# Optimization experiments

Hardware: AMD Instinct MI355X
Metric: run time of the kernel (lower is better)

The kernel has to match this reference:

```python
import jax, jax.numpy as jnp
import numpy as np

MODES, WIDTH, DEPTH, IN_F, OUT_F, HID = 8, 16, 3, 1, 1, 64


def setup_inputs() -> dict:
    key = jax.random.key(0)
    ks = jax.random.split(key, 12)
    B, H, W = 8, 512, 512
    scale = 1.0 / (WIDTH * WIDTH)
    inp = {
        'x': jax.random.normal(ks[0], (B, IN_F, H, W), dtype=jnp.float32),
        'fc0_w': jax.random.normal(ks[1], (IN_F, WIDTH), dtype=jnp.float32) * 0.5,
        'fc0_b': jax.random.normal(ks[2], (WIDTH,), dtype=jnp.float32) * 0.1,
        # complex spectral weights stored as real/imag parts, stacked over depth
        'spec_wr': jax.random.normal(ks[3], (DEPTH, WIDTH, WIDTH, MODES, MODES), dtype=jnp.float32) * scale,
        'spec_wi': jax.random.normal(ks[4], (DEPTH, WIDTH, WIDTH, MODES, MODES), dtype=jnp.float32) * scale,
        # 1x1 convs as [depth, out, in] matmuls + bias
        'conv_w': jax.random.normal(ks[5], (DEPTH, WIDTH, WIDTH), dtype=jnp.float32) * 0.25,
        'conv_b': jax.random.normal(ks[6], (DEPTH, WIDTH), dtype=jnp.float32) * 0.1,
        'fc1_w': jax.random.normal(ks[7], (WIDTH, HID), dtype=jnp.float32) * 0.25,
        'fc1_b': jax.random.normal(ks[8], (HID,), dtype=jnp.float32) * 0.1,
        'fc2_w': jax.random.normal(ks[9], (HID, OUT_F), dtype=jnp.float32) * 0.125,
        'fc2_b': jax.random.normal(ks[10], (OUT_F,), dtype=jnp.float32) * 0.1,
    }
    return inp


def _spectral_conv(x, w):
    # x: [B, Ci, H, W] real; w: [Ci, Co, m, m] complex
    B, C, H, W = x.shape
    m = w.shape[2]
    x_ft = jnp.fft.rfft2(x, norm='forward')  # [B, Ci, H, W//2+1]
    out_modes = jnp.einsum('bixy,ioxy->boxy', x_ft[:, :, :m, :m], w)
    out_ft = jnp.zeros((B, w.shape[1], H, W // 2 + 1), dtype=out_modes.dtype)
    out_ft = out_ft.at[:, :, :m, :m].set(out_modes)
    return jnp.fft.irfft2(out_ft, s=(H, W), norm='forward')


def reference(x, fc0_w, fc0_b, spec_wr, spec_wi, conv_w, conv_b, fc1_w, fc1_b, fc2_w, fc2_b):
    # lift: [B,C,H,W] -> channels-last linear -> [B,width,H,W]
    h = jnp.einsum('bchw,cd->bdhw', x, fc0_w) + fc0_b[None, :, None, None]
    for d in range(DEPTH):
        w_c = (spec_wr[d] + 1j * spec_wi[d]).astype(jnp.complex64)
        y = _spectral_conv(h, w_c)
        local = jnp.einsum('bchw,oc->bohw', h, conv_w[d]) + conv_b[d][None, :, None, None]
        h = y + local
    h = jnp.einsum('bchw,cd->bdhw', h, fc1_w) + fc1_b[None, :, None, None]
    h = jax.nn.relu(h)
    out = jnp.einsum('bchw,cd->bdhw', h, fc2_w) + fc2_b[None, :, None, None]
    return out
```

## Files before the change

kernel.cpp:

```cpp
#include <hip/hip_runtime.h>
#include <math.h>

#define NB 8
#define NH 512
#define NW 512
#define ANG512 0.01227184630308513f
#define SPEC_D 16384

typedef __attribute__((ext_vector_type(8))) _Float16 f16x8;
typedef __attribute__((ext_vector_type(4))) float    f32x4;

__global__ __launch_bounds__(256) void k_pre(const float* __restrict__ x,
                                             float* __restrict__ P) {
    __shared__ float wred[8][16];
    const int tid = threadIdx.x;
    const int w = tid >> 6, lane = tid & 63;
    const int gid = blockIdx.x;
    const int b = gid >> 6, rg = gid & 63;

    #pragma unroll
    for (int rr = 0; rr < 2; ++rr) {
        const int row = rg * 8 + w + 4 * rr;
        const float* xr = x + ((size_t)(b * NH + row)) * NW;

        float p[16];
        #pragma unroll
        for (int j = 0; j < 16; ++j) p[j] = 0.f;

        #pragma unroll
        for (int j = 0; j < 4; ++j) {
            const int ww = lane + (j << 6);
            const float xa = xr[ww], xb = xr[ww + 256];
            const float a = xa + xb, d = xa - xb;
            float c1, s1;
            __sincosf(ANG512 * (float)ww, &s1, &c1);
            p[0] += a;
            p[1] = fmaf(d, c1, p[1]);
            p[9] = fmaf(-d, s1, p[9]);
            const float c2k = 2.f * c1;
            float ckm = 1.f, skm = 0.f, ck = c1, sk = s1;
            #pragma unroll
            for (int k = 2; k < 8; ++k) {
                const float cn = fmaf(c2k, ck, -ckm);
                const float sn = fmaf(c2k, sk, -skm);
                ckm = ck; skm = sk; ck = cn; sk = sn;
                const float v = (k & 1) ? d : a;
                p[k]     = fmaf(v, ck, p[k]);
                p[8 + k] = fmaf(-v, sk, p[8 + k]);
            }
        }
        #pragma unroll
        for (int m = 1; m < 64; m <<= 1) {
            #pragma unroll
            for (int j = 0; j < 16; ++j) p[j] += __shfl_xor(p[j], m);
        }
        if (lane < 16) wred[w + 4 * rr][lane] = p[lane];
    }
    __syncthreads();

    if (tid < 128) {
        const int kx = tid >> 4, q = tid & 15, qm = q & 7;
        float acc = 0.f;
        #pragma unroll
        for (int r = 0; r < 8; ++r) {
            const int row = rg * 8 + r;
            const int m = (kx * row) & 511;
            float cm, s2;
            __sincosf(ANG512 * (float)m, &s2, &cm);
            const float rre = wred[r][qm], rim = wred[r][8 + qm];
            acc += (q < 8) ? (rre * cm + rim * s2)
                           : (rim * cm - rre * s2);
        }
        P[((size_t)((b * 64 + rg) * 8 + kx)) * 16 + q] = acc;
    }
}

__global__ __launch_bounds__(256) void k_modes(
        const float* __restrict__ P,
        const float* __restrict__ spec_wr, const float* __restrict__ spec_wi,
        const float* __restrict__ conv_w, const float* __restrict__ conv_b,
        const float* __restrict__ fc0_w, const float* __restrict__ fc0_b,
        const float* __restrict__ fc1_w, const float* __restrict__ fc1_b,
        float* __restrict__ AH, float* __restrict__ gv, float* __restrict__ Kv) {
    __shared__ __align__(16) float sm[2640];
    float* red2  = sm;
    float* X2    = sm + 256;
    float* Xr    = sm + 272;
    float* Xi    = sm + 400;
    float* Fr    = sm + 528;
    float* Fi    = sm + 656;
    float* Ar    = sm + 784;
    float* Ai    = sm + 912;
    float* Pm    = sm + 1040;
    float* fc1_s = sm + 1552;
    float* ps    = sm + 2576;

    const int tid = threadIdx.x;
    const int bid = blockIdx.x;
    const int b = bid >> 3;
    const int kx = bid & 7;

    {
        const int o = tid >> 4, c = tid & 15;
        float s = 0.f;
        for (int k = 0; k < 16; ++k)
            s += conv_w[512 + o * 16 + k] * conv_w[256 + k * 16 + c];
        Pm[tid] = s;
    }
    Pm[256 + tid] = conv_w[512 + tid];
    #pragma unroll
    for (int k = 0; k < 4; ++k) fc1_s[tid + k * 256] = fc1_w[tid + k * 256];

    {
        const int q = tid & 15, c = tid >> 4;
        float acc = 0.f;
        #pragma unroll
        for (int m = 0; m < 4; ++m) {
            const int rg = c + 16 * m;
            acc += P[((size_t)((b * 64 + rg) * 8 + kx)) * 16 + q];
        }
        red2[c * 16 + q] = acc;
    }
    __syncthreads();
    if (tid < 16) {
        float s = 0.f;
        #pragma unroll
        for (int c = 0; c < 16; ++c) s += red2[c * 16 + tid];
        X2[tid] = s;
    }
    __syncthreads();

    const bool act = (tid < 128);
    const int o = tid >> 3, ky = tid & 7;
    if (act) {
        const float inv = 1.f / (512.f * 512.f);
        float xr0 = fc0_w[o] * X2[ky] * inv;
        float xi0 = fc0_w[o] * X2[8 + ky] * inv;
        if (kx == 0 && ky == 0) xr0 += fc0_b[o];
        Xr[o * 8 + ky] = xr0; Xi[o * 8 + ky] = xi0;
        Ar[o * 8 + ky] = 0.f; Ai[o * 8 + ky] = 0.f;
    }
    __syncthreads();

    for (int dd = 0; dd < 3; ++dd) {
        if (act) {
            float fr = 0.f, fi = 0.f;
            const float* wrp = spec_wr + (size_t)dd * SPEC_D + o * 64 + kx * 8 + ky;
            const float* wip = spec_wi + (size_t)dd * SPEC_D + o * 64 + kx * 8 + ky;
            #pragma unroll
            for (int i = 0; i < 16; ++i) {
                const float wre = wrp[i * 1024];
                const float wim = wip[i * 1024];
                const float xr0 = Xr[i * 8 + ky], xi0 = Xi[i * 8 + ky];
                fr += xr0 * wre - xi0 * wim;
                fi += xr0 * wim + xi0 * wre;
            }
            Fr[o * 8 + ky] = fr; Fi[o * 8 + ky] = fi;
        }
        __syncthreads();
        float xnr = 0.f, xni = 0.f;
        if (act) {
            float ar, ai;
            if (dd == 2) {
                ar = Fr[o * 8 + ky]; ai = Fi[o * 8 + ky];
            } else {
                ar = 0.f; ai = 0.f;
                #pragma unroll
                for (int c = 0; c < 16; ++c) {
                    const float pv = Pm[dd * 256 + o * 16 + c];
                    ar = fmaf(pv, Fr[c * 8 + ky], ar);
                    ai = fmaf(pv, Fi[c * 8 + ky], ai);
                }
            }
            Ar[o * 8 + ky] += ar; Ai[o * 8 + ky] += ai;
            if (dd < 2) {
                const float fr0 = Fr[o * 8 + ky], fi0 = Fi[o * 8 + ky];
                if (ky == 0) {
                    if (kx == 0) { xnr = fr0; xni = 0.f; }
                    else         { xnr = 0.5f * fr0; xni = 0.5f * fi0; }
                } else { xnr = fr0; xni = fi0; }
                #pragma unroll
                for (int c = 0; c < 16; ++c) {
                    const float cc = conv_w[dd * 256 + o * 16 + c];
                    xnr = fmaf(cc, Xr[c * 8 + ky], xnr);
                    xni = fmaf(cc, Xi[c * 8 + ky], xni);
                }
                if (kx == 0 && ky == 0) xnr += conv_b[dd * 16 + o];
            }
        }
        __syncthreads();
        if (act && dd < 2) { Xr[o * 8 + ky] = xnr; Xi[o * 8 + ky] = xni; }
        __syncthreads();
    }

    #pragma unroll
    for (int k2 = 0; k2 < 2; ++k2) {
        const int idx = tid + k2 * 256;
        const int hd = idx >> 3, ky2 = idx & 7;
        float ar = 0.f, ai = 0.f;
        #pragma unroll
        for (int c = 0; c < 16; ++c) {
            const float f = fc1_s[c * 64 + hd];
            ar = fmaf(f, Ar[c * 8 + ky2], ar);
            ai = fmaf(f, Ai[c * 8 + ky2], ai);
        }
        const float ck = (ky2 == 0) ? 1.f : 2.f;
        const size_t off = ((((size_t)(b * 64 + hd)) * 8 + ky2) * 8 + kx) * 2;
        AH[off]     = ck * ar;
        AH[off + 1] = ck * ai;
    }

    if (kx == 0) {
        if (tid < 16) {
            float su = 0.f, sb = 0.f;
            for (int c = 0; c < 16; ++c) {
                su += conv_w[tid * 16 + c] * fc0_w[c];
                sb += conv_w[tid * 16 + c] * fc0_b[c];
            }
            ps[tid] = su; ps[16 + tid] = sb;
        }
        __syncthreads();
        if (tid < 16) {
            float dv = 0.f, ev = conv_b[32 + tid];
            for (int k = 0; k < 16; ++k) {
                dv += Pm[tid * 16 + k] * ps[k];
                ev += Pm[tid * 16 + k] * (ps[16 + k] + conv_b[k]);
                ev += conv_w[512 + tid * 16 + k] * conv_b[16 + k];
            }
            ps[32 + tid] = dv; ps[48 + tid] = ev;
        }
        __syncthreads();
        if (tid < 64) {
            float g = 0.f, K = fc1_b[tid];
            for (int c = 0; c < 16; ++c) {
                g = fmaf(fc1_w[c * 64 + tid], ps[32 + c], g);
                K = fmaf(fc1_w[c * 64 + tid], ps[48 + c], K);
            }
            gv[b * 64 + tid] = g;
            Kv[b * 64 + tid] = K;
        }
    }
}

__global__ __launch_bounds__(256, 4) void k_head(
        const float* __restrict__ x, const float* __restrict__ AH,
        const float* __restrict__ gv, const float* __restrict__ Kv,
        const float* __restrict__ fc2_w, const float* __restrict__ fc2_b,
        float* __restrict__ out) {
    __shared__ __align__(16) _Float16 Ef[2][512][8];
    __shared__ __align__(16) _Float16 Apk[4][4][64][8];

    const int tid  = threadIdx.x;
    const int lane = tid & 63;
    const int rl   = tid >> 6;
    const int b    = blockIdx.x >> 7;
    const int rp   = blockIdx.x & 127;
    const int row  = rp * 4 + rl;

    #pragma unroll
    for (int pxi = 0; pxi < 2; ++pxi) {
        const int px = tid + pxi * 256;
        float c1, s1;
        __sincosf(ANG512 * (float)px, &s1, &c1);
        float ck = 1.f, sk = 0.f;
        #pragma unroll
        for (int k = 0; k < 8; ++k) {
            Ef[0][px][k] = (_Float16)ck;
            Ef[1][px][k] = (_Float16)(-sk);
            const float cn = ck * c1 - sk * s1;
            const float sn = sk * c1 + ck * s1;
            ck = cn; sk = sn;
        }
    }

    float ghr[16], w2r[16];
    {
        const int lg = lane >> 4;
        #pragma unroll
        for (int t = 0; t < 4; ++t)
            #pragma unroll
            for (int v = 0; v < 4; ++v) {
                const int hd = t * 16 + lg * 4 + v;
                ghr[t * 4 + v] = gv[b * 64 + hd];
                w2r[t * 4 + v] = fc2_w[hd];
            }
    }

    {
        float c1, s1;
        __sincosf(ANG512 * (float)row, &s1, &c1);
        float ctr[8], str[8];
        ctr[0] = 1.f; str[0] = 0.f; ctr[1] = c1; str[1] = s1;
        const float c2k = 2.f * c1;
        #pragma unroll
        for (int k = 2; k < 8; ++k) {
            ctr[k] = fmaf(c2k, ctr[k - 1], -ctr[k - 2]);
            str[k] = fmaf(c2k, str[k - 1], -str[k - 2]);
        }
        #pragma unroll
        for (int j = 0; j < 8; ++j) {
            const int idx = lane + j * 64;
            const int hd = idx >> 3, ky = idx & 7;
            const float4* ap = (const float4*)(AH + ((size_t)(b * 64 + hd) * 8 + ky) * 16);
            const float4 a0 = ap[0], a1 = ap[1], a2 = ap[2], a3 = ap[3];
            float wr = a0.x, wi = a0.y;
            wr = fmaf(a0.z, ctr[1], wr); wr = fmaf(-a0.w, str[1], wr);
            wi = fmaf(a0.z, str[1], wi); wi = fmaf(a0.w, ctr[1], wi);
            wr = fmaf(a1.x, ctr[2], wr); wr = fmaf(-a1.y, str[2], wr);
            wi = fmaf(a1.x, str[2], wi); wi = fmaf(a1.y, ctr[2], wi);
            wr = fmaf(a1.z, ctr[3], wr); wr = fmaf(-a1.w, str[3], wr);
            wi = fmaf(a1.z, str[3], wi); wi = fmaf(a1.w, ctr[3], wi);
            wr = fmaf(a2.x, ctr[4], wr); wr = fmaf(-a2.y, str[4], wr);
            wi = fmaf(a2.x, str[4], wi); wi = fmaf(a2.y, ctr[4], wi);
            wr = fmaf(a2.z, ctr[5], wr); wr = fmaf(-a2.w, str[5], wr);
            wi = fmaf(a2.z, str[5], wi); wi = fmaf(a2.w, ctr[5], wi);
            wr = fmaf(a3.x, ctr[6], wr); wr = fmaf(-a3.y, str[6], wr);
            wi = fmaf(a3.x, str[6], wi); wi = fmaf(a3.y, ctr[6], wi);
            wr = fmaf(a3.z, ctr[7], wr); wr = fmaf(-a3.w, str[7], wr);
            wi = fmaf(a3.w, ctr[7], wi); wi = fmaf(a3.z, str[7], wi);
            if (ky == 0) wr += Kv[b * 64 + hd];
            const _Float16 hr  = (_Float16)wr;
            const _Float16 hi_ = (_Float16)wi;
            Apk[rl][0][hd][ky] = hr;
            Apk[rl][1][hd][ky] = hi_;
            Apk[rl][2][hd][ky] = (_Float16)(wr - (float)hr);
            Apk[rl][3][hd][ky] = (_Float16)(wi - (float)hi_);
        }
    }
    __syncthreads();

    f16x8 a1[4];
    {
        const int kb = lane >> 4, m = lane & 15;
        #pragma unroll
        for (int t = 0; t < 4; ++t)
            a1[t] = *(const f16x8*)&Apk[rl][kb][t * 16 + m][0];
    }

    const int eb = (lane >> 4) & 1, n = lane & 15;
    const float fc2b = fc2_b[0];
    const float* xrow = x + ((size_t)(b * NH + row)) * NW;
    float* orow = out + ((size_t)(b * NH + row)) * NW;

    #pragma unroll 2
    for (int pxt = 0; pxt < 32; ++pxt) {
        const int px = pxt * 16 + n;
        const f16x8 b1 = *(const f16x8*)&Ef[eb][px][0];
        f32x4 c[4];
        #pragma unroll
        for (int t = 0; t < 4; ++t) {
            c[t] = (f32x4){0.f, 0.f, 0.f, 0.f};
            c[t] = __builtin_amdgcn_mfma_f32_16x16x32_f16(a1[t], b1, c[t], 0, 0, 0);
        }
        const float xpx = xrow[px];
        float val = 0.f;
        #pragma unroll
        for (int t = 0; t < 4; ++t)
            #pragma unroll
            for (int v = 0; v < 4; ++v) {
                float s = fmaf(ghr[t * 4 + v], xpx, c[t][v]);
                s = fmaxf(s, 0.f);
                val = fmaf(s, w2r[t * 4 + v], val);
            }
        val += __shfl_xor(val, 16);
        val += __shfl_xor(val, 32);
        if (lane < 16) orow[pxt * 16 + lane] = val + fc2b;
    }
}

extern "C" void kernel_launch(void* const* d_in, const int* in_sizes, int n_in,
                              void* d_out, int out_size, void* d_ws, size_t ws_size,
                              hipStream_t stream) {
    const float* x       = (const float*)d_in[0];
    const float* fc0_w   = (const float*)d_in[1];
    const float* fc0_b   = (const float*)d_in[2];
    const float* spec_wr = (const float*)d_in[3];
    const float* spec_wi = (const float*)d_in[4];
    const float* conv_w  = (const float*)d_in[5];
    const float* conv_b  = (const float*)d_in[6];
    const float* fc1_w   = (const float*)d_in[7];
    const float* fc1_b   = (const float*)d_in[8];
    const float* fc2_w   = (const float*)d_in[9];
    const float* fc2_b   = (const float*)d_in[10];
    float* outp = (float*)d_out;

    char* ws = (char*)d_ws;
    float* P  = (float*)ws;
    float* AH = (float*)(ws + 262144);
    float* gv = (float*)(ws + 524288);
    float* Kv = (float*)(ws + 526336);

    k_pre<<<512, 256, 0, stream>>>(x, P);
    k_modes<<<64, 256, 0, stream>>>(P, spec_wr, spec_wi, conv_w, conv_b,
                                    fc0_w, fc0_b, fc1_w, fc1_b, AH, gv, Kv);
    k_head<<<1024, 256, 0, stream>>>(x, AH, gv, Kv, fc2_w, fc2_b, outp);
}
```

Before: 118.0 us.

## Fuse pre-reduction and mode kernels via device-scope atomic counters; prefetch in head

Result: slower. 121.3 us (+2.8%).

```diff
diff --git a/kernel.cpp b/kernel.cpp
--- a/kernel.cpp
+++ b/kernel.cpp
@@ -7,237 +7,266 @@
 #define ANG512 0.01227184630308513f
 #define SPEC_D 16384
 
+#define DEV_SCOPE __HIP_MEMORY_SCOPE_AGENT
+
 typedef __attribute__((ext_vector_type(8))) _Float16 f16x8;
 typedef __attribute__((ext_vector_type(4))) float    f32x4;
 
-__global__ __launch_bounds__(256) void k_pre(const float* __restrict__ x,
-                                             float* __restrict__ P) {
-    __shared__ float wred[8][16];
+__device__ int g_pre[256];
+__device__ int g_done[256];
+
+__global__ __launch_bounds__(256) void k_front(
+        const float* __restrict__ x,
+        const float* __restrict__ spec_wr, const float* __restrict__ spec_wi,
+        const float* __restrict__ conv_w, const float* __restrict__ conv_b,
+        const float* __restrict__ fc0_w, const float* __restrict__ fc0_b,
+        const float* __restrict__ fc1_w, const float* __restrict__ fc1_b,
+        float* __restrict__ P, float* __restrict__ AH,
+        float* __restrict__ gv, float* __restrict__ Kv) {
+    __shared__ __align__(16) float sm[2640];
     const int tid = threadIdx.x;
     const int w = tid >> 6, lane = tid & 63;
     const int gid = blockIdx.x;
     const int b = gid >> 6, rg = gid & 63;
 
-    #pragma unroll
-    for (int rr = 0; rr < 2; ++rr) {
-        const int row = rg * 8 + w + 4 * rr;
-        const float* xr = x + ((size_t)(b * NH + row)) * NW;
-
-        float p[16];
-        #pragma unroll
-        for (int j = 0; j < 16; ++j) p[j] = 0.f;
-
-        #pragma unroll
-        for (int j = 0; j < 4; ++j) {
-            const int ww = lane + (j << 6);
-            const float xa = xr[ww], xb = xr[ww + 256];
-            const float a = xa + xb, d = xa - xb;
-            float c1, s1;
-            __sincosf(ANG512 * (float)ww, &s1, &c1);
-            p[0] += a;
-            p[1] = fmaf(d, c1, p[1]);
-            p[9] = fmaf(-d, s1, p[9]);
-            const float c2k = 2.f * c1;
-            float ckm = 1.f, skm = 0.f, ck = c1, sk = s1;
-            #pragma unroll
-            for (int k = 2; k < 8; ++k) {
-                const float cn = fmaf(c2k, ck, -ckm);
-                const float sn = fmaf(c2k, sk, -skm);
-                ckm = ck; skm = sk; ck = cn; sk = sn;
-                const float v = (k & 1) ? d : a;
-                p[k]     = fmaf(v, ck, p[k]);
-                p[8 + k] = fmaf(-v, sk, p[8 + k]);
-            }
-        }
-        #pragma unroll
-        for (int m = 1; m < 64; m <<= 1) {
-            #pragma unroll
-            for (int j = 0; j < 16; ++j) p[j] += __shfl_xor(p[j], m);
-        }
-        if (lane < 16) wred[w + 4 * rr][lane] = p[lane];
-    }
-    __syncthreads();
-
-    if (tid < 128) {
-        const int kx = tid >> 4, q = tid & 15, qm = q & 7;
-        float acc = 0.f;
-        #pragma unroll
-        for (int r = 0; r < 8; ++r) {
-            const int row = rg * 8 + r;
-            const int m = (kx * row) & 511;
-            float cm, s2;
-            __sincosf(ANG512 * (float)m, &s2, &cm);
-            const float rre = wred[r][qm], rim = wred[r][8 + qm];
-            acc += (q < 8) ? (rre * cm + rim * s2)
-                           : (rim * cm - rre * s2);
-        }
-        P[((size_t)((b * 64 + rg) * 8 + kx)) * 16 + q] = acc;
-    }
-}
-
-__global__ __launch_bounds__(256) void k_modes(
-        const float* __restrict__ P,
-        const float* __restrict__ spec_wr, const float* __restrict__ spec_wi,
-        const float* __restrict__ conv_w, const float* __restrict__ conv_b,
-        const float* __restrict__ fc0_w, const float* __restrict__ fc0_b,
-        const float* __restrict__ fc1_w, const float* __restrict__ fc1_b,
-        float* __restrict__ AH, float* __restrict__ gv, float* __restrict__ Kv) {
-    __shared__ __align__(16) float sm[2640];
-    float* red2  = sm;
-    float* X2    = sm + 256;
-    float* Xr    = sm + 272;
-    float* Xi    = sm + 400;
-    float* Fr    = sm + 528;
-    float* Fi    = sm + 656;
-    float* Ar    = sm + 784;
-    float* Ai    = sm + 912;
-    float* Pm    = sm + 1040;
-    float* fc1_s = sm + 1552;
-    float* ps    = sm + 2576;
-
-    const int tid = threadIdx.x;
-    const int bid = blockIdx.x;
-    const int b = bid >> 3;
-    const int kx = bid & 7;
-
     {
-        const int o = tid >> 4, c = tid & 15;
-        float s = 0.f;
-        for (int k = 0; k < 16; ++k)
-            s += conv_w[512 + o * 16 + k] * conv_w[256 + k * 16 + c];
-        Pm[tid] = s;
-    }
-    Pm[256 + tid] = conv_w[512 + tid];
-    #pragma unroll
-    for (int k = 0; k < 4; ++k) fc1_s[tid + k * 256] = fc1_w[tid + k * 256];
+        float* wred = sm;
+        #pragma unroll
+        for (int rr = 0; rr < 2; ++rr) {
+            const int row = rg * 8 + w + 4 * rr;
+            const float* xr = x + ((size_t)(b * NH + row)) * NW;
+
+            float p[16];
+            #pragma unroll
+            for (int j = 0; j < 16; ++j) p[j] = 0.f;
+
+            #pragma unroll
+            for (int j = 0; j < 4; ++j) {
+                const int ww = lane + (j << 6);
+                const float xa = xr[ww], xb = xr[ww + 256];
+                const float a = xa + xb, d = xa - xb;
+                float c1, s1;
+                __sincosf(ANG512 * (float)ww, &s1, &c1);
+                p[0] += a;
+                p[1] = fmaf(d, c1, p[1]);
+                p[9] = fmaf(-d, s1, p[9]);
+                const float c2k = 2.f * c1;
+                float ckm = 1.f, skm = 0.f, ck = c1, sk = s1;
+                #pragma unroll
+                for (int k = 2; k < 8; ++k) {
+                    const float cn = fmaf(c2k, ck, -ckm);
+                    const float sn = fmaf(c2k, sk, -skm);
+                    ckm = ck; skm = sk; ck = cn; sk = sn;
+                    const float v = (k & 1) ? d : a;
+                    p[k]     = fmaf(v, ck, p[k]);
+                    p[8 + k] = fmaf(-v, sk, p[8 + k]);
+                }
+            }
+            #pragma unroll
+            for (int m = 1; m < 64; m <<= 1) {
+                #pragma unroll
+                for (int j = 0; j < 16; ++j) p[j] += __shfl_xor(p[j], m);
+            }
+            if (lane < 16) wred[(w + 4 * rr) * 16 + lane] = p[lane];
+        }
+        __syncthreads();
+
+        if (tid < 128) {
+            const int kx = tid >> 4, q = tid & 15, qm = q & 15 & 7;
+            float acc = 0.f;
+            #pragma unroll
+            for (int r = 0; r < 8; ++r) {
+                const int row = rg * 8 + r;
+                const int m = (kx * row) & 511;
+                float cm, s2;
+                __sincosf(ANG512 * (float)m, &s2, &cm);
+                const float rre = wred[r * 16 + qm], rim = wred[r * 16 + 8 + qm];
+                acc += (q < 8) ? (rre * cm + rim * s2)
+                               : (rim * cm - rre * s2);
+            }
+            __hip_atomic_store(&P[((size_t)((b * 64 + rg) * 8 + kx)) * 16 + q],
+                               acc, __ATOMIC_RELAXED, DEV_SCOPE);
+        }
+        __syncthreads();
+        if (tid == 0)
+            __hip_atomic_fetch_add(&g_pre[b * 32], 1, __ATOMIC_RELEASE, DEV_SCOPE);
+    }
+
+    if (gid >= 64) return;
 
     {
-        const int q = tid & 15, c = tid >> 4;
-        float acc = 0.f;
-        #pragma unroll
-        for (int m = 0; m < 4; ++m) {
-            const int rg = c + 16 * m;
-            acc += P[((size_t)((b * 64 + rg) * 8 + kx)) * 16 + q];
-        }
-        red2[c * 16 + q] = acc;
-    }
-    __syncthreads();
-    if (tid < 16) {
-        float s = 0.f;
-        #pragma unroll
-        for (int c = 0; c < 16; ++c) s += red2[c * 16 + tid];
-        X2[tid] = s;
-    }
-    __syncthreads();
-
-    const bool act = (tid < 128);
-    const int o = tid >> 3, ky = tid & 7;
-    if (act) {
-        const float inv = 1.f / (512.f * 512.f);
-        float xr0 = fc0_w[o] * X2[ky] * inv;
-        float xi0 = fc0_w[o] * X2[8 + ky] * inv;
-        if (kx == 0 && ky == 0) xr0 += fc0_b[o];
-        Xr[o * 8 + ky] = xr0; Xi[o * 8 + ky] = xi0;
-        Ar[o * 8 + ky] = 0.f; Ai[o * 8 + ky] = 0.f;
-    }
-    __syncthreads();
-
-    for (int dd = 0; dd < 3; ++dd) {
+        float* red2  = sm;
+        float* X2    = sm + 256;
+        float* Xr    = sm + 272;
+        float* Xi    = sm + 400;
+        float* Fr    = sm + 528;
+        float* Fi    = sm + 656;
+        float* Ar    = sm + 784;
+        float* Ai    = sm + 912;
+        float* Pm    = sm + 1040;
+        float* fc1_s = sm + 1552;
+        float* ps    = sm + 2576;
+
+        const int b2 = gid >> 3;
+        const int kx = gid & 7;
+
+        __syncthreads();
+
+        {
+            const int o = tid >> 4, c = tid & 15;
+            float s = 0.f;
+            for (int k = 0; k < 16; ++k)
+                s += conv_w[512 + o * 16 + k] * conv_w[256 + k * 16 + c];
+            Pm[tid] = s;
+        }
+        Pm[256 + tid] = conv_w[512 + tid];
+        #pragma unroll
+        for (int k = 0; k < 4; ++k) fc1_s[tid + k * 256] = fc1_w[tid + k * 256];
+
+        if (tid == 0) {
+            while (__hip_atomic_load(&g_pre[b2 * 32], __ATOMIC_RELAXED, DEV_SCOPE) < 64)
+                __builtin_amdgcn_s_sleep(2);
+        }
+        __syncthreads();
+
+        {
+            const int q = tid & 15, c = tid >> 4;
+            float acc = 0.f;
+            #pragma unroll
+            for (int m = 0; m < 4; ++m) {
+                const int rg2 = c + 16 * m;
+                acc += P[((size_t)((b2 * 64 + rg2) * 8 + kx)) * 16 + q];
+            }
+            red2[c * 16 + q] = acc;
+        }
+        __syncthreads();
+        if (tid < 16) {
+            float s = 0.f;
+            #pragma unroll
+            for (int c = 0; c < 16; ++c) s += red2[c * 16 + tid];
+            X2[tid] = s;
+        }
+        __syncthreads();
+
+        const bool act = (tid < 128);
+        const int o = tid >> 3, ky = tid & 7;
         if (act) {
-            float fr = 0.f, fi = 0.f;
-            const float* wrp = spec_wr + (size_t)dd * SPEC_D + o * 64 + kx * 8 + ky;
-            const float* wip = spec_wi + (size_t)dd * SPEC_D + o * 64 + kx * 8 + ky;
-            #pragma unroll
-            for (int i = 0; i < 16; ++i) {
-                const float wre = wrp[i * 1024];
-                const float wim = wip[i * 1024];
-                const float xr0 = Xr[i * 8 + ky], xi0 = Xi[i * 8 + ky];
-                fr += xr0 * wre - xi0 * wim;
-                fi += xr0 * wim + xi0 * wre;
-            }
-            Fr[o * 8 + ky] = fr; Fi[o * 8 + ky] = fi;
-        }
-        __syncthreads();
-        float xnr = 0.f, xni = 0.f;
-        if (act) {
-            float ar, ai;
-            if (dd == 2) {
-                ar = Fr[o * 8 + ky]; ai = Fi[o * 8 + ky];
-            } else {
-                ar = 0.f; ai = 0.f;
+            const float inv = 1.f / (512.f * 512.f);
+            float xr0 = fc0_w[o] * X2[ky] * inv;
+            float xi0 = fc0_w[o] * X2[8 + ky] * inv;
+            if (kx == 0 && ky == 0) xr0 += fc0_b[o];
+            Xr[o * 8 + ky] = xr0; Xi[o * 8 + ky] = xi0;
+            Ar[o * 8 + ky] = 0.f; Ai[o * 8 + ky] = 0.f;
+        }
+        __syncthreads();
+
+        for (int dd = 0; dd < 3; ++dd) {
+            if (act) {
+                float fr = 0.f, fi = 0.f;
+                const float* wrp = spec_wr + (size_t)dd * SPEC_D + o * 64 + kx * 8 + ky;
+                const float* wip = spec_wi + (size_t)dd * SPEC_D + o * 64 + kx * 8 + ky;
                 #pragma unroll
+                for (int i = 0; i < 16; ++i) {
+                    const float wre = wrp[i * 1024];
+                    const float wim = wip[i * 1024];
+                    const float xr0 = Xr[i * 8 + ky], xi0 = Xi[i * 8 + ky];
+                    fr += xr0 * wre - xi0 * wim;
+                    fi += xr0 * wim + xi0 * wre;
+                }
+                Fr[o * 8 + ky] = fr; Fi[o * 8 + ky] = fi;
+            }
+            __syncthreads();
+            float xnr = 0.f, xni = 0.f;
+            if (act) {
+                float ar, ai;
+                if (dd == 2) {
+                    ar = Fr[o * 8 + ky]; ai = Fi[o * 8 + ky];
+                } else {
+                    ar = 0.f; ai = 0.f;
+                    #pragma unroll
+                    for (int c = 0; c < 16; ++c) {
+                        const float pv = Pm[dd * 256 + o * 16 + c];
+                        ar = fmaf(pv, Fr[c * 8 + ky], ar);
+                        ai = fmaf(pv, Fi[c * 8 + ky], ai);
+                    }
+                }
+                Ar[o * 8 + ky] += ar; Ai[o * 8 + ky] += ai;
+                if (dd < 2) {
+                    const float fr0 = Fr[o * 8 + ky], fi0 = Fi[o * 8 + ky];
+                    if (ky == 0) {
+                        if (kx == 0) { xnr = fr0; xni = 0.f; }
+                        else         { xnr = 0.5f * fr0; xni = 0.5f * fi0; }
+                    } else { xnr = fr0; xni = fi0; }
+                    #pragma unroll
+                    for (int c = 0; c < 16; ++c) {
+                        const float cc = conv_w[dd * 256 + o * 16 + c];
+                        xnr = fmaf(cc, Xr[c * 8 + ky], xnr);
+                        xni = fmaf(cc, Xi[c * 8 + ky], xni);
+                    }
+                    if (kx == 0 && ky == 0) xnr += conv_b[dd * 16 + o];
+                }
+            }
+            __syncthreads();
+            if (act && dd < 2) { Xr[o * 8 + ky] = xnr; Xi[o * 8 + ky] = xni; }
+            __syncthreads();
+        }
+
+        #pragma unroll
+        for (int k2 = 0; k2 < 2; ++k2) {
+            const int idx = tid + k2 * 256;
+            const int hd = idx >> 3, ky2 = idx & 7;
+            float ar = 0.f, ai = 0.f;
+            #pragma unroll
+            for (int c = 0; c < 16; ++c) {
+                const float f = fc1_s[c * 64 + hd];
+                ar = fmaf(f, Ar[c * 8 + ky2], ar);
+                ai = fmaf(f, Ai[c * 8 + ky2], ai);
+            }
+            const float ck = (ky2 == 0) ? 1.f : 2.f;
+            const size_t off = ((((size_t)(b2 * 64 + hd)) * 8 + ky2) * 8 + kx) * 2;
+            AH[off]     = ck * ar;
+            AH[off + 1] = ck * ai;
+        }
+
+        if (kx == 0) {
+            if (tid < 16) {
+                float su = 0.f, sb = 0.f;
                 for (int c = 0; c < 16; ++c) {
-                    const float pv = Pm[dd * 256 + o * 16 + c];
-                    ar = fmaf(pv, Fr[c * 8 + ky], ar);
-                    ai = fmaf(pv, Fi[c * 8 + ky], ai);
-                }
-            }
-            Ar[o * 8 + ky] += ar; Ai[o * 8 + ky] += ai;
-            if (dd < 2) {
-                const float fr0 = Fr[o * 8 + ky], fi0 = Fi[o * 8 + ky];
-                if (ky == 0) {
-                    if (kx == 0) { xnr = fr0; xni = 0.f; }
-                    else         { xnr = 0.5f * fr0; xni = 0.5f * fi0; }
-                } else { xnr = fr0; xni = fi0; }
-                #pragma unroll
+                    su += conv_w[tid * 16 + c] * fc0_w[c];
+                    sb += conv_w[tid * 16 + c] * fc0_b[c];
+                }
+                ps[tid] = su; ps[16 + tid] = sb;
+            }
+            __syncthreads();
+            if (tid < 16) {
+                float dv = 0.f, ev = conv_b[32 + tid];
+                for (int k = 0; k < 16; ++k) {
+                    dv += Pm[tid * 16 + k] * ps[k];
+                    ev += Pm[tid * 16 + k] * (ps[16 + k] + conv_b[k]);
+                    ev += conv_w[512 + tid * 16 + k] * conv_b[16 + k];
+                }
+                ps[32 + tid] = dv; ps[48 + tid] = ev;
+            }
+            __syncthreads();
+            if (tid < 64) {
+                float g = 0.f, K = fc1_b[tid];
                 for (int c = 0; c < 16; ++c) {
-                    const float cc = conv_w[dd * 256 + o * 16 + c];
-                    xnr = fmaf(cc, Xr[c * 8 + ky], xnr);
-                    xni = fmaf(cc, Xi[c * 8 + ky], xni);
-                }
-                if (kx == 0 && ky == 0) xnr += conv_b[dd * 16 + o];
-            }
-        }
-        __syncthreads();
-        if (act && dd < 2) { Xr[o * 8 + ky] = xnr; Xi[o * 8 + ky] = xni; }
-        __syncthreads();
-    }
-
-    #pragma unroll
-    for (int k2 = 0; k2 < 2; ++k2) {
-        const int idx = tid + k2 * 256;
-        const int hd = idx >> 3, ky2 = idx & 7;
-        float ar = 0.f, ai = 0.f;
-        #pragma unroll
-        for (int c = 0; c < 16; ++c) {
-            const float f = fc1_s[c * 64 + hd];
-            ar = fmaf(f, Ar[c * 8 + ky2], ar);
-            ai = fmaf(f, Ai[c * 8 + ky2], ai);
-        }
-        const float ck = (ky2 == 0) ? 1.f : 2.f;
-        const size_t off = ((((size_t)(b * 64 + hd)) * 8 + ky2) * 8 + kx) * 2;
-        AH[off]     = ck * ar;
-        AH[off + 1] = ck * ai;
-    }
-
-    if (kx == 0) {
-        if (tid < 16) {
-            float su = 0.f, sb = 0.f;
-            for (int c = 0; c < 16; ++c) {
-                su += conv_w[tid * 16 + c] * fc0_w[c];
-                sb += conv_w[tid * 16 + c] * fc0_b[c];
-            }
-            ps[tid] = su; ps[16 + tid] = sb;
-        }
-        __syncthreads();
-        if (tid < 16) {
-            float dv = 0.f, ev = conv_b[32 + tid];
-            for (int k = 0; k < 16; ++k) {
-                dv += Pm[tid * 16 + k] * ps[k];
-                ev += Pm[tid * 16 + k] * (ps[16 + k] + conv_b[k]);
-                ev += conv_w[512 + tid * 16 + k] * conv_b[16 + k];
-            }
-            ps[32 + tid] = dv; ps[48 + tid] = ev;
-        }
-        __syncthreads();
-        if (tid < 64) {
-            float g = 0.f, K = fc1_b[tid];
-            for (int c = 0; c < 16; ++c) {
-                g = fmaf(fc1_w[c * 64 + tid], ps[32 + c], g);
-                K = fmaf(fc1_w[c * 64 + tid], ps[48 + c], K);
-            }
-            gv[b * 64 + tid] = g;
-            Kv[b * 64 + tid] = K;
+                    g = fmaf(fc1_w[c * 64 + tid], ps[32 + c], g);
+                    K = fmaf(fc1_w[c * 64 + tid], ps[48 + c], K);
+                }
+                gv[b2 * 64 + tid] = g;
+                Kv[b2 * 64 + tid] = K;
+            }
+        }
+
+        __syncthreads();
+        if (tid == 0) {
+            const int d = __hip_atomic_fetch_add(&g_done[b2 * 32], 1,
+                                                 __ATOMIC_RELAXED, DEV_SCOPE);
+            if (d == 7) {
+                __hip_atomic_store(&g_pre[b2 * 32],  0, __ATOMIC_RELAXED, DEV_SCOPE);
+                __hip_atomic_store(&g_done[b2 * 32], 0, __ATOMIC_RELAXED, DEV_SCOPE);
+            }
         }
     }
 }
@@ -342,17 +371,23 @@
     const float* xrow = x + ((size_t)(b * NH + row)) * NW;
     float* orow = out + ((size_t)(b * NH + row)) * NW;
 
-    #pragma unroll 2
+    f16x8 bnext = *(const f16x8*)&Ef[eb][n][0];
+    float xnext = xrow[n];
+
+    #pragma unroll 4
     for (int pxt = 0; pxt < 32; ++pxt) {
-        const int px = pxt * 16 + n;
-        const f16x8 b1 = *(const f16x8*)&Ef[eb][px][0];
+        const f16x8 b1 = bnext;
+        const float xpx = xnext;
+        if (pxt < 31) {
+            bnext = *(const f16x8*)&Ef[eb][(pxt + 1) * 16 + n][0];
+            xnext = xrow[(pxt + 1) * 16 + n];
+        }
         f32x4 c[4];
         #pragma unroll
         for (int t = 0; t < 4; ++t) {
             c[t] = (f32x4){0.f, 0.f, 0.f, 0.f};
             c[t] = __builtin_amdgcn_mfma_f32_16x16x32_f16(a1[t], b1, c[t], 0, 0, 0);
         }
-        const float xpx = xrow[px];
         float val = 0.f;
         #pragma unroll
         for (int t = 0; t < 4; ++t)
@@ -390,8 +425,7 @@
     float* gv = (float*)(ws + 524288);
     float* Kv = (float*)(ws + 526336);
 
-    k_pre<<<512, 256, 0, stream>>>(x, P);
-    k_modes<<<64, 256, 0, stream>>>(P, spec_wr, spec_wi, conv_w, conv_b,
-                                    fc0_w, fc0_b, fc1_w, fc1_b, AH, gv, Kv);
+    k_front<<<512, 256, 0, stream>>>(x, spec_wr, spec_wi, conv_w, conv_b,
+                                     fc0_w, fc0_b, fc1_w, fc1_b, P, AH, gv, Kv);
     k_head<<<1024, 256, 0, stream>>>(x, AH, gv, Kv, fc2_w, fc2_b, outp);
 }
```

## Split k_head rows across two waves per row with software-prefetched loop

Applied to the files above, without the earlier changes.

Measured after the change: 182.0 us. 54.3% more time.

```diff
diff --git a/kernel.cpp b/kernel.cpp
--- a/kernel.cpp
+++ b/kernel.cpp
@@ -242,7 +242,7 @@
     }
 }
 
-__global__ __launch_bounds__(256, 4) void k_head(
+__global__ __launch_bounds__(512, 8) void k_head(
         const float* __restrict__ x, const float* __restrict__ AH,
         const float* __restrict__ gv, const float* __restrict__ Kv,
         const float* __restrict__ fc2_w, const float* __restrict__ fc2_b,
@@ -252,14 +252,15 @@
 
     const int tid  = threadIdx.x;
     const int lane = tid & 63;
-    const int rl   = tid >> 6;
+    const int wid  = tid >> 6;
+    const int rl   = wid >> 1;
+    const int h    = wid & 1;
     const int b    = blockIdx.x >> 7;
     const int rp   = blockIdx.x & 127;
     const int row  = rp * 4 + rl;
 
-    #pragma unroll
-    for (int pxi = 0; pxi < 2; ++pxi) {
-        const int px = tid + pxi * 256;
+    {
+        const int px = tid;
         float c1, s1;
         __sincosf(ANG512 * (float)px, &s1, &c1);
         float ck = 1.f, sk = 0.f;
@@ -298,8 +299,8 @@
             str[k] = fmaf(c2k, str[k - 1], -str[k - 2]);
         }
         #pragma unroll
-        for (int j = 0; j < 8; ++j) {
-            const int idx = lane + j * 64;
+        for (int j = 0; j < 4; ++j) {
+            const int idx = lane + (h * 4 + j) * 64;
             const int hd = idx >> 3, ky = idx & 7;
             const float4* ap = (const float4*)(AH + ((size_t)(b * 64 + hd) * 8 + ky) * 16);
             const float4 a0 = ap[0], a1 = ap[1], a2 = ap[2], a3 = ap[3];
@@ -341,30 +342,39 @@
     const float fc2b = fc2_b[0];
     const float* xrow = x + ((size_t)(b * NH + row)) * NW;
     float* orow = out + ((size_t)(b * NH + row)) * NW;
-
-    #pragma unroll 2
-    for (int pxt = 0; pxt < 32; ++pxt) {
-        const int px = pxt * 16 + n;
-        const f16x8 b1 = *(const f16x8*)&Ef[eb][px][0];
+    const int tl0 = h * 16;
+
+    f16x8 bn = *(const f16x8*)&Ef[eb][tl0 * 16 + n][0];
+    float xn = xrow[tl0 * 16 + n];
+
+    #pragma unroll 4
+    for (int it = 0; it < 16; ++it) {
+        const f16x8 b1 = bn;
+        const float xpx = xn;
+        if (it < 15) {
+            const int p = (tl0 + it + 1) * 16 + n;
+            bn = *(const f16x8*)&Ef[eb][p][0];
+            xn = xrow[p];
+        }
         f32x4 c[4];
         #pragma unroll
         for (int t = 0; t < 4; ++t) {
             c[t] = (f32x4){0.f, 0.f, 0.f, 0.f};
             c[t] = __builtin_amdgcn_mfma_f32_16x16x32_f16(a1[t], b1, c[t], 0, 0, 0);
         }
-        const float xpx = xrow[px];
-        float val = 0.f;
+        float p4[4] = {0.f, 0.f, 0.f, 0.f};
         #pragma unroll
         for (int t = 0; t < 4; ++t)
             #pragma unroll
             for (int v = 0; v < 4; ++v) {
                 float s = fmaf(ghr[t * 4 + v], xpx, c[t][v]);
                 s = fmaxf(s, 0.f);
-                val = fmaf(s, w2r[t * 4 + v], val);
-            }
+                p4[v] = fmaf(s, w2r[t * 4 + v], p4[v]);
+            }
+        float val = (p4[0] + p4[1]) + (p4[2] + p4[3]);
         val += __shfl_xor(val, 16);
         val += __shfl_xor(val, 32);
-        if (lane < 16) orow[pxt * 16 + lane] = val + fc2b;
+        if (lane < 16) orow[(tl0 + it) * 16 + lane] = val + fc2b;
     }
 }
 
@@ -393,5 +403,5 @@
     k_pre<<<512, 256, 0, stream>>>(x, P);
     k_modes<<<64, 256, 0, stream>>>(P, spec_wr, spec_wi, conv_w, conv_b,
                                     fc0_w, fc0_b, fc1_w, fc1_b, AH, gv, Kv);
-    k_head<<<1024, 256, 0, stream>>>(x, AH, gv, Kv, fc2_w, fc2_b, outp);
+    k_head<<<1024, 512, 0, stream>>>(x, AH, gv, Kv, fc2_w, fc2_b, outp);
 }
```
